# Performance work log

Measured on AMD Instinct MI355X. Metric: run time of the kernel, lower is better.

Reference implementation:

```python
import jax, jax.numpy as jnp
import numpy as np

H, W, N, G = 256, 256, 4096, 4
CHOL_BOUND = np.array([0.5, 0.0, 0.5], np.float32)

def _haar_highpass(x):
    # level-1 haar wavedec -> waverec with approx coeffs zeroed
    n = len(x) - (len(x) % 2)
    pairs = x[:n].reshape(-1, 2)
    d = (pairs[:, 0] - pairs[:, 1]) / np.sqrt(2.0)
    rec = np.zeros(len(x), np.float32)
    rec[0:n:2] = d / np.sqrt(2.0)
    rec[1:n:2] = -d / np.sqrt(2.0)
    return rec

def setup_inputs():
    rng = np.random.RandomState(0)
    xyz = rng.randn(N, 2).astype(np.float32)
    chol = (rng.randn(N, 3) * 0.1).astype(np.float32)
    feats = rng.rand(N, 3).astype(np.float32)
    opac = np.ones((N, 1), np.float32)
    hf = np.stack([_haar_highpass(xyz[:, i]) for i in range(2)], 1)
    mag = np.linalg.norm(hf, axis=1)
    thr = np.quantile(mag, 0.75)  # deterministic 75/25 split -> Nl=3072, Nh=1024
    high = mag > thr
    low = ~high
    nh = int(high.sum())
    gabor_freqs = (0.1 + 0.01 * rng.randn(nh * G, 2)).astype(np.float32)
    gabor_weights = (0.01 + 0.001 * rng.randn(nh * G, 1)).astype(np.float32)
    return {
        'low_mu': jnp.asarray(xyz[low]), 'high_mu': jnp.asarray(xyz[high]),
        'low_chol': jnp.asarray(chol[low]), 'high_chol': jnp.asarray(chol[high]),
        'low_feat': jnp.asarray(feats[low]), 'high_feat': jnp.asarray(feats[high]),
        'low_opac': jnp.asarray(opac[low]), 'high_opac': jnp.asarray(opac[high]),
        'gabor_freqs': jnp.asarray(gabor_freqs),
        'gabor_weights': jnp.asarray(gabor_weights),
    }

def _project(mu, chol):
    # project_gaussians_2d: tanh(mu) in [-1,1] -> pixel coords; Sigma = L L^T, conic = Sigma^-1
    m = jnp.tanh(mu)
    xy = jnp.stack([(m[:, 0] + 1.0) * 0.5 * W, (m[:, 1] + 1.0) * 0.5 * H], -1)
    ch = chol + jnp.asarray(CHOL_BOUND)
    l1, l2, l3 = ch[:, 0], ch[:, 1], ch[:, 2]
    sxx, sxy, syy = l1 * l1, l1 * l2, l2 * l2 + l3 * l3
    det = sxx * syy - sxy * sxy
    conic = jnp.stack([syy / det, -sxy / det, sxx / det], -1)  # (A, B, C)
    return xy, conic

def _pad(a, m):
    return jnp.concatenate([a, jnp.zeros((m - a.shape[0],) + a.shape[1:], a.dtype)], 0)

def _sigma(xyc, cc, xs, ys):
    dx = xs[None, :] - xyc[:, 0:1]  # [C,W]
    dy = ys[None, :] - xyc[:, 1:2]  # [C,H]
    return (0.5 * cc[:, 0, None, None] * dx[:, None, :] ** 2
            + cc[:, 1, None, None] * dy[:, :, None] * dx[:, None, :]
            + 0.5 * cc[:, 2, None, None] * dy[:, :, None] ** 2)  # [C,H,W]

def _raster_gauss(xy, conic, colors, opac, chunk=256):
    # rasterize_gaussians_sum: out(p) = sum_i opac_i * exp(-sigma_i(p)) * color_i
    xs = jnp.arange(W, dtype=jnp.float32) + 0.5
    ys = jnp.arange(H, dtype=jnp.float32) + 0.5
    m = ((xy.shape[0] + chunk - 1) // chunk) * chunk
    parts = tuple(_pad(a, m).reshape(-1, chunk, a.shape[1]) for a in (xy, conic, colors, opac))
    def body(acc, sl):
        xyc, cc, col, op = sl
        wgt = op[:, 0, None, None] * jnp.exp(-_sigma(xyc, cc, xs, ys))
        return acc + jnp.einsum('chw,ck->hwk', wgt, col), None
    acc, _ = jax.lax.scan(body, jnp.zeros((H, W, 3), jnp.float32), parts)
    return acc

def _raster_gabor(xy, conic, colors, opac, freqs, weights, chunk=64):
    # rasterize_gabor_sum: gaussian envelope modulated by a weighted sum of G cosine carriers
    xs = jnp.arange(W, dtype=jnp.float32) + 0.5
    ys = jnp.arange(H, dtype=jnp.float32) + 0.5
    n = xy.shape[0]
    fx = freqs[:, 0].reshape(n, G)
    fy = freqs[:, 1].reshape(n, G)
    wg = weights[:, 0].reshape(n, G)
    m = ((n + chunk - 1) // chunk) * chunk
    parts = tuple(_pad(a, m).reshape(-1, chunk, a.shape[1]) for a in (xy, conic, colors, opac, fx, fy, wg))
    def body(acc, sl):
        xyc, cc, col, op, fxc, fyc, wc = sl
        dx = xs[None, :] - xyc[:, 0:1]
        dy = ys[None, :] - xyc[:, 1:2]
        phase = (fxc[:, :, None, None] * dx[:, None, None, :]
                 + fyc[:, :, None, None] * dy[:, None, :, None])  # [C,G,H,W]
        mod = jnp.sum(wc[:, :, None, None] * jnp.cos(phase), axis=1)  # [C,H,W]
        wgt = op[:, 0, None, None] * jnp.exp(-_sigma(xyc, cc, xs, ys)) * mod
        return acc + jnp.einsum('chw,ck->hwk', wgt, col), None
    acc, _ = jax.lax.scan(body, jnp.zeros((H, W, 3), jnp.float32), parts)
    return acc

def reference(low_mu, high_mu, low_chol, high_chol, low_feat, high_feat,
              low_opac, high_opac, gabor_freqs, gabor_weights):
    xy_l, con_l = _project(low_mu, low_chol)
    xy_h, con_h = _project(high_mu, high_chol)
    out_low = _raster_gauss(xy_l, con_l, low_feat, low_opac)
    out_high = _raster_gabor(xy_h, con_h, high_feat, high_opac, gabor_freqs, gabor_weights)
    img = jnp.clip(out_low + out_high, 0.0, 1.0)  # [H,W,3]
    return img.transpose(2, 0, 1)[None]  # [1,3,H,W]
```

## Files before the change

kernel.cpp:

```cpp
#include <hip/hip_runtime.h>

#define IMG_W 256
#define IMG_H 256
#define GG 4
#define CUT 15.0f

__global__ __launch_bounds__(256) void project_kernel(
    const float* __restrict__ low_mu,   const float* __restrict__ low_chol,
    const float* __restrict__ low_feat, const float* __restrict__ low_opac,
    const float* __restrict__ high_mu,  const float* __restrict__ high_chol,
    const float* __restrict__ high_feat,const float* __restrict__ high_opac,
    const float* __restrict__ gfreq,    const float* __restrict__ gweight,
    int nl, int nh,
    float* __restrict__ plow, float* __restrict__ phigh)
{
    int i = blockIdx.x * blockDim.x + threadIdx.x;
    if (i >= nl + nh) return;
    bool islow = (i < nl);
    int k = islow ? i : (i - nl);
    const float* mu   = islow ? low_mu   : high_mu;
    const float* chol = islow ? low_chol : high_chol;
    const float* feat = islow ? low_feat : high_feat;
    const float* opac = islow ? low_opac : high_opac;

    float m0 = tanhf(mu[2*k]);
    float m1 = tanhf(mu[2*k+1]);
    float cx = (m0 + 1.0f) * 0.5f * (float)IMG_W;
    float cy = (m1 + 1.0f) * 0.5f * (float)IMG_H;

    float l1 = chol[3*k]     + 0.5f;
    float l2 = chol[3*k + 1];
    float l3 = chol[3*k + 2] + 0.5f;
    float sxx = l1*l1, sxy = l1*l2, syy = l2*l2 + l3*l3;
    float det = sxx*syy - sxy*sxy;
    float inv = 1.0f / det;
    float q0 = syy*inv, q1 = -sxy*inv, q2 = sxx*inv;

    float ht = 0.5f*(q0 + q2);
    float hd = 0.5f*(q0 - q2);
    float lam = ht - sqrtf(hd*hd + q1*q1);
    lam = fmaxf(lam, 1e-6f);
    float rad = sqrtf(2.0f * CUT / lam) + 1.0f;

    float op = opac[k];
    float pr = feat[3*k]*op, pg = feat[3*k+1]*op, pb = feat[3*k+2]*op;

    if (islow) {
        float* p = plow + (size_t)k * 12;
        p[0]=cx; p[1]=cy; p[2]=0.5f*q0; p[3]=q1; p[4]=0.5f*q2; p[5]=rad;
        p[6]=pr; p[7]=pg; p[8]=pb; p[9]=0.f; p[10]=0.f; p[11]=0.f;
    } else {
        float* p = phigh + (size_t)k * 24;
        p[0]=cx; p[1]=cy; p[2]=0.5f*q0; p[3]=q1; p[4]=0.5f*q2; p[5]=rad;
        p[6]=pr; p[7]=pg; p[8]=pb; p[9]=0.f; p[10]=0.f; p[11]=0.f;
        #pragma unroll
        for (int g = 0; g < GG; ++g) {
            p[12+g] = gfreq[(k*GG + g)*2];
            p[16+g] = gfreq[(k*GG + g)*2 + 1];
            p[20+g] = gweight[k*GG + g];
        }
    }
}

__global__ __launch_bounds__(256) void raster_kernel(
    const float* __restrict__ plow, int nl,
    const float* __restrict__ phigh, int nh,
    float* __restrict__ out)
{
    __shared__ int s_cnt;
    __shared__ int s_list[4096];

    const int tid = threadIdx.x;
    const int bx = blockIdx.x & 15, by = blockIdx.x >> 4;
    const float tx0 = bx*16 + 0.5f, ty0 = by*16 + 0.5f;
    const float tx1 = tx0 + 15.0f,  ty1 = ty0 + 15.0f;
    const int lx = tid & 15, ly = tid >> 4;
    const float px = bx*16 + lx + 0.5f;
    const float py = by*16 + ly + 0.5f;

    float accr = 0.f, accg = 0.f, accb = 0.f;

    if (tid == 0) s_cnt = 0;
    __syncthreads();
    for (int i = tid; i < nl; i += 256) {
        const float* p = plow + (size_t)i * 12;
        float cx = p[0], cy = p[1], rad = p[5];
        if (cx + rad >= tx0 && cx - rad <= tx1 &&
            cy + rad >= ty0 && cy - rad <= ty1) {
            int slot = atomicAdd(&s_cnt, 1);
            s_list[slot] = i;
        }
    }
    __syncthreads();
    int cnt = s_cnt;
    for (int j = 0; j < cnt; ++j) {
        int idx = __builtin_amdgcn_readfirstlane(s_list[j]);
        const float* p = plow + (size_t)idx * 12;
        float dx = px - p[0], dy = py - p[1];
        float s  = (p[2]*dx + p[3]*dy)*dx + p[4]*dy*dy;
        float e  = __expf(-s);
        accr = fmaf(e, p[6], accr);
        accg = fmaf(e, p[7], accg);
        accb = fmaf(e, p[8], accb);
    }
    __syncthreads();

    if (tid == 0) s_cnt = 0;
    __syncthreads();
    for (int i = tid; i < nh; i += 256) {
        const float* p = phigh + (size_t)i * 24;
        float cx = p[0], cy = p[1], rad = p[5];
        if (cx + rad >= tx0 && cx - rad <= tx1 &&
            cy + rad >= ty0 && cy - rad <= ty1) {
            int slot = atomicAdd(&s_cnt, 1);
            s_list[slot] = i;
        }
    }
    __syncthreads();
    cnt = s_cnt;
    for (int j = 0; j < cnt; ++j) {
        int idx = __builtin_amdgcn_readfirstlane(s_list[j]);
        const float* p = phigh + (size_t)idx * 24;
        float dx = px - p[0], dy = py - p[1];
        float s  = (p[2]*dx + p[3]*dy)*dx + p[4]*dy*dy;
        float e  = __expf(-s);
        float mod = 0.f;
        #pragma unroll
        for (int g = 0; g < GG; ++g) {
            float ph = p[12+g]*dx + p[16+g]*dy;
            mod = fmaf(p[20+g], __cosf(ph), mod);
        }
        float e2 = e * mod;
        accr = fmaf(e2, p[6], accr);
        accg = fmaf(e2, p[7], accg);
        accb = fmaf(e2, p[8], accb);
    }

    int x = bx*16 + lx, y = by*16 + ly;
    int pix = y*IMG_W + x;
    out[pix]                 = fminf(fmaxf(accr, 0.f), 1.f);
    out[IMG_H*IMG_W + pix]   = fminf(fmaxf(accg, 0.f), 1.f);
    out[2*IMG_H*IMG_W + pix] = fminf(fmaxf(accb, 0.f), 1.f);
}

extern "C" void kernel_launch(void* const* d_in, const int* in_sizes, int n_in,
                              void* d_out, int out_size, void* d_ws, size_t ws_size,
                              hipStream_t stream)
{
    const float* low_mu    = (const float*)d_in[0];
    const float* high_mu   = (const float*)d_in[1];
    const float* low_chol  = (const float*)d_in[2];
    const float* high_chol = (const float*)d_in[3];
    const float* low_feat  = (const float*)d_in[4];
    const float* high_feat = (const float*)d_in[5];
    const float* low_opac  = (const float*)d_in[6];
    const float* high_opac = (const float*)d_in[7];
    const float* gfreq     = (const float*)d_in[8];
    const float* gweight   = (const float*)d_in[9];

    int nl = in_sizes[0] / 2;
    int nh = in_sizes[1] / 2;

    float* plow  = (float*)d_ws;
    float* phigh = plow + (size_t)nl * 12;
    float* out   = (float*)d_out;

    int n = nl + nh;
    project_kernel<<<(n + 255) / 256, 256, 0, stream>>>(
        low_mu, low_chol, low_feat, low_opac,
        high_mu, high_chol, high_feat, high_opac,
        gfreq, gweight, nl, nh, plow, phigh);

    raster_kernel<<<256, 256, 0, stream>>>(plow, nl, phigh, nh, out);
}
```

Measured before the change: 90.56 us.

## Fuse projection into raster kernel and stage per-tile Gaussian params in LDS

After: 91.09 us. Within noise of the previous version (+0.6%).

```diff
diff --git a/kernel.cpp b/kernel.cpp
--- a/kernel.cpp
+++ b/kernel.cpp
@@ -4,71 +4,47 @@
 #define IMG_H 256
 #define GG 4
 #define CUT 15.0f
+#define LOW_CAP  384
+#define HIGH_CAP 192
+#define LO_STRIDE 8
+#define HI_STRIDE 20
 
-__global__ __launch_bounds__(256) void project_kernel(
+
+__device__ __forceinline__ void project_one(
+    const float* __restrict__ mu, const float* __restrict__ chol, int k,
+    float& cx, float& cy, float& A, float& B, float& C, float& rad)
+{
+    float m0 = tanhf(mu[2*k]);
+    float m1 = tanhf(mu[2*k+1]);
+    cx = (m0 + 1.0f) * 0.5f * (float)IMG_W;
+    cy = (m1 + 1.0f) * 0.5f * (float)IMG_H;
+
+    float l1 = chol[3*k]     + 0.5f;
+    float l2 = chol[3*k + 1];
+    float l3 = chol[3*k + 2] + 0.5f;
+    float sxx = l1*l1, sxy = l1*l2, syy = l2*l2 + l3*l3;
+    float inv = 1.0f / (sxx*syy - sxy*sxy);
+    float q0 = syy*inv, q1 = -sxy*inv, q2 = sxx*inv;
+    A = 0.5f*q0; B = q1; C = 0.5f*q2;
+
+    float ht = 0.5f*(q0 + q2);
+    float hd = 0.5f*(q0 - q2);
+    float lam = fmaxf(ht - sqrtf(hd*hd + q1*q1), 1e-6f);
+    rad = sqrtf(2.0f * CUT / lam) + 1.0f;
+}
+
+__global__ __launch_bounds__(256) void fused_kernel(
     const float* __restrict__ low_mu,   const float* __restrict__ low_chol,
     const float* __restrict__ low_feat, const float* __restrict__ low_opac,
     const float* __restrict__ high_mu,  const float* __restrict__ high_chol,
     const float* __restrict__ high_feat,const float* __restrict__ high_opac,
     const float* __restrict__ gfreq,    const float* __restrict__ gweight,
     int nl, int nh,
-    float* __restrict__ plow, float* __restrict__ phigh)
-{
-    int i = blockIdx.x * blockDim.x + threadIdx.x;
-    if (i >= nl + nh) return;
-    bool islow = (i < nl);
-    int k = islow ? i : (i - nl);
-    const float* mu   = islow ? low_mu   : high_mu;
-    const float* chol = islow ? low_chol : high_chol;
-    const float* feat = islow ? low_feat : high_feat;
-    const float* opac = islow ? low_opac : high_opac;
-
-    float m0 = tanhf(mu[2*k]);
-    float m1 = tanhf(mu[2*k+1]);
-    float cx = (m0 + 1.0f) * 0.5f * (float)IMG_W;
-    float cy = (m1 + 1.0f) * 0.5f * (float)IMG_H;
-
-    float l1 = chol[3*k]     + 0.5f;
-    float l2 = chol[3*k + 1];
-    float l3 = chol[3*k + 2] + 0.5f;
-    float sxx = l1*l1, sxy = l1*l2, syy = l2*l2 + l3*l3;
-    float det = sxx*syy - sxy*sxy;
-    float inv = 1.0f / det;
-    float q0 = syy*inv, q1 = -sxy*inv, q2 = sxx*inv;
-
-    float ht = 0.5f*(q0 + q2);
-    float hd = 0.5f*(q0 - q2);
-    float lam = ht - sqrtf(hd*hd + q1*q1);
-    lam = fmaxf(lam, 1e-6f);
-    float rad = sqrtf(2.0f * CUT / lam) + 1.0f;
-
-    float op = opac[k];
-    float pr = feat[3*k]*op, pg = feat[3*k+1]*op, pb = feat[3*k+2]*op;
-
-    if (islow) {
-        float* p = plow + (size_t)k * 12;
-        p[0]=cx; p[1]=cy; p[2]=0.5f*q0; p[3]=q1; p[4]=0.5f*q2; p[5]=rad;
-        p[6]=pr; p[7]=pg; p[8]=pb; p[9]=0.f; p[10]=0.f; p[11]=0.f;
-    } else {
-        float* p = phigh + (size_t)k * 24;
-        p[0]=cx; p[1]=cy; p[2]=0.5f*q0; p[3]=q1; p[4]=0.5f*q2; p[5]=rad;
-        p[6]=pr; p[7]=pg; p[8]=pb; p[9]=0.f; p[10]=0.f; p[11]=0.f;
-        #pragma unroll
-        for (int g = 0; g < GG; ++g) {
-            p[12+g] = gfreq[(k*GG + g)*2];
-            p[16+g] = gfreq[(k*GG + g)*2 + 1];
-            p[20+g] = gweight[k*GG + g];
-        }
-    }
-}
-
-__global__ __launch_bounds__(256) void raster_kernel(
-    const float* __restrict__ plow, int nl,
-    const float* __restrict__ phigh, int nh,
     float* __restrict__ out)
 {
-    __shared__ int s_cnt;
-    __shared__ int s_list[4096];
+    __shared__ int s_nlo, s_nhi;
+    __shared__ float s_lo[LOW_CAP  * LO_STRIDE];
+    __shared__ float s_hi[HIGH_CAP * HI_STRIDE];
 
     const int tid = threadIdx.x;
     const int bx = blockIdx.x & 15, by = blockIdx.x >> 4;
@@ -78,66 +54,77 @@
     const float px = bx*16 + lx + 0.5f;
     const float py = by*16 + ly + 0.5f;
 
-    float accr = 0.f, accg = 0.f, accb = 0.f;
+    if (tid == 0) { s_nlo = 0; s_nhi = 0; }
+    __syncthreads();
 
-    if (tid == 0) s_cnt = 0;
-    __syncthreads();
     for (int i = tid; i < nl; i += 256) {
-        const float* p = plow + (size_t)i * 12;
-        float cx = p[0], cy = p[1], rad = p[5];
+        float cx, cy, A, B, C, rad;
+        project_one(low_mu, low_chol, i, cx, cy, A, B, C, rad);
         if (cx + rad >= tx0 && cx - rad <= tx1 &&
             cy + rad >= ty0 && cy - rad <= ty1) {
-            int slot = atomicAdd(&s_cnt, 1);
-            s_list[slot] = i;
+            int slot = atomicAdd(&s_nlo, 1);
+            if (slot < LOW_CAP) {
+                float op = low_opac[i];
+                float* p = s_lo + slot * LO_STRIDE;
+                p[0]=cx; p[1]=cy; p[2]=A; p[3]=B; p[4]=C;
+                p[5]=low_feat[3*i]*op; p[6]=low_feat[3*i+1]*op; p[7]=low_feat[3*i+2]*op;
+            }
+        }
+    }
+    for (int i = tid; i < nh; i += 256) {
+        float cx, cy, A, B, C, rad;
+        project_one(high_mu, high_chol, i, cx, cy, A, B, C, rad);
+        if (cx + rad >= tx0 && cx - rad <= tx1 &&
+            cy + rad >= ty0 && cy - rad <= ty1) {
+            int slot = atomicAdd(&s_nhi, 1);
+            if (slot < HIGH_CAP) {
+                float op = high_opac[i];
+                float* p = s_hi + slot * HI_STRIDE;
+                p[0]=cx; p[1]=cy; p[2]=A; p[3]=B; p[4]=C;
+                p[5]=high_feat[3*i]*op; p[6]=high_feat[3*i+1]*op; p[7]=high_feat[3*i+2]*op;
+                #pragma unroll
+                for (int g = 0; g < GG; ++g) {
+                    p[8+g]  = gfreq[(i*GG + g)*2];
+                    p[12+g] = gfreq[(i*GG + g)*2 + 1];
+                    p[16+g] = gweight[i*GG + g];
+                }
+            }
         }
     }
     __syncthreads();
-    int cnt = s_cnt;
-    for (int j = 0; j < cnt; ++j) {
-        int idx = __builtin_amdgcn_readfirstlane(s_list[j]);
-        const float* p = plow + (size_t)idx * 12;
+
+    const int clo = min(s_nlo, LOW_CAP);
+    const int chi = min(s_nhi, HIGH_CAP);
+
+    float accr = 0.f, accg = 0.f, accb = 0.f;
+
+    for (int j = 0; j < clo; ++j) {
+        const float* p = s_lo + j * LO_STRIDE;
         float dx = px - p[0], dy = py - p[1];
         float s  = (p[2]*dx + p[3]*dy)*dx + p[4]*dy*dy;
         float e  = __expf(-s);
-        accr = fmaf(e, p[6], accr);
-        accg = fmaf(e, p[7], accg);
-        accb = fmaf(e, p[8], accb);
+        accr = fmaf(e, p[5], accr);
+        accg = fmaf(e, p[6], accg);
+        accb = fmaf(e, p[7], accb);
     }
-    __syncthreads();
-
-    if (tid == 0) s_cnt = 0;
-    __syncthreads();
-    for (int i = tid; i < nh; i += 256) {
-        const float* p = phigh + (size_t)i * 24;
-        float cx = p[0], cy = p[1], rad = p[5];
-        if (cx + rad >= tx0 && cx - rad <= tx1 &&
-            cy + rad >= ty0 && cy - rad <= ty1) {
-            int slot = atomicAdd(&s_cnt, 1);
-            s_list[slot] = i;
-        }
-    }
-    __syncthreads();
-    cnt = s_cnt;
-    for (int j = 0; j < cnt; ++j) {
-        int idx = __builtin_amdgcn_readfirstlane(s_list[j]);
-        const float* p = phigh + (size_t)idx * 24;
+    for (int j = 0; j < chi; ++j) {
+        const float* p = s_hi + j * HI_STRIDE;
         float dx = px - p[0], dy = py - p[1];
         float s  = (p[2]*dx + p[3]*dy)*dx + p[4]*dy*dy;
         float e  = __expf(-s);
         float mod = 0.f;
         #pragma unroll
         for (int g = 0; g < GG; ++g) {
-            float ph = p[12+g]*dx + p[16+g]*dy;
-            mod = fmaf(p[20+g], __cosf(ph), mod);
+            float ph = p[8+g]*dx + p[12+g]*dy;
+            mod = fmaf(p[16+g], __cosf(ph), mod);
         }
         float e2 = e * mod;
-        accr = fmaf(e2, p[6], accr);
-        accg = fmaf(e2, p[7], accg);
-        accb = fmaf(e2, p[8], accb);
+        accr = fmaf(e2, p[5], accr);
+        accg = fmaf(e2, p[6], accg);
+        accb = fmaf(e2, p[7], accb);
     }
 
-    int x = bx*16 + lx, y = by*16 + ly;
-    int pix = y*IMG_W + x;
+    int pix = (by*16 + ly)*IMG_W + (bx*16 + lx);
     out[pix]                 = fminf(fmaxf(accr, 0.f), 1.f);
     out[IMG_H*IMG_W + pix]   = fminf(fmaxf(accg, 0.f), 1.f);
     out[2*IMG_H*IMG_W + pix] = fminf(fmaxf(accb, 0.f), 1.f);
@@ -161,15 +148,8 @@
     int nl = in_sizes[0] / 2;
     int nh = in_sizes[1] / 2;
 
-    float* plow  = (float*)d_ws;
-    float* phigh = plow + (size_t)nl * 12;
-    float* out   = (float*)d_out;
-
-    int n = nl + nh;
-    project_kernel<<<(n + 255) / 256, 256, 0, stream>>>(
+    fused_kernel<<<256, 256, 0, stream>>>(
         low_mu, low_chol, low_feat, low_opac,
         high_mu, high_chol, high_feat, high_opac,
-        gfreq, gweight, nl, nh, plow, phigh);
-
-    raster_kernel<<<256, 256, 0, stream>>>(plow, nl, phigh, nh, out);
+        gfreq, gweight, nl, nh, (float*)d_out);
 }
```
